# Kernel optimization log

Hardware: AMD Instinct MI355X
Metric: run time of the kernel (lower is better)

Reference implementation:

```python
import jax, jax.numpy as jnp
import numpy as np

D_MODEL = 512
D_STATE = 64
L_SEQ = 4096
BATCH = 4


def _make_A(N):
    # HiPPO-LegS style A: A[n,k] = -sqrt(2n+1)sqrt(2k+1) if n>k, -(n+1) if n==k, 0 else (n,k from 1..N)
    idx = np.arange(1, N + 1, dtype=np.float64)
    M = np.sqrt(2 * idx[:, None] + 1) * np.sqrt(2 * idx[None, :] + 1)
    lower = (idx[:, None] > idx[None, :]).astype(np.float64)
    return -(lower * M + np.diag(idx + 1))


def _discretize(A, B, C, step):
    # bilinear (Tustin) transform
    I = np.eye(A.shape[0])
    BL = np.linalg.inv(I - step / 2.0 * A)
    Ab = BL @ (I + step / 2.0 * A)
    Bb = (BL * step) @ B
    return Ab, Bb, C


def setup_inputs() -> dict:
    key = jax.random.key(0)
    rng = np.random.RandomState(0)
    A = _make_A(D_STATE)
    B = rng.randn(D_STATE, 1)
    C = rng.randn(1, D_STATE)
    Ab, Bb, Cb = _discretize(A, B, C, step=1.0 / L_SEQ)
    u = jax.random.normal(key, (BATCH, L_SEQ, D_MODEL), dtype=jnp.float32)
    return {
        "u": u,
        "A_": jnp.asarray(Ab, dtype=jnp.float32),
        "B_": jnp.asarray(Bb, dtype=jnp.float32),
        "C_": jnp.asarray(Cb, dtype=jnp.float32),
    }


def reference(u, A_, B_, C_):
    # u: (B, L, D) -> flatten channels: (BD, L)
    b, L, d = u.shape
    uc = u.transpose(0, 2, 1).reshape(b * d, L)
    N = A_.shape[0]
    b_vec = B_[:, 0]  # (N,)
    c_vec = C_[0]     # (N,)

    def step(x, u_k):
        # x: (BD, N), u_k: (BD,)
        # x_k = A_ @ x_{k-1}^T + B_ @ u_k^T  (expressed batched as x @ A_.T + outer)
        x_new = x @ A_.T + u_k[:, None] * b_vec[None, :]
        y_k = x_new @ c_vec  # (BD,)
        return x_new, y_k

    x0 = jnp.zeros((b * d, N), dtype=u.dtype)
    _, ys = jax.lax.scan(step, x0, uc.T)  # ys: (L, BD)
    y = ys.T.reshape(b, d, L).transpose(0, 2, 1)  # (B, L, D)
    return y
```

## Files before the change

### kernel.cpp

```cpp
#include <hip/hip_runtime.h>

#define L_SEQ   4096
#define D_MODEL 512
#define NSEQ    2048
#define CH      128
#define NC      32

#define OFF_P    0
#define OFF_W1T  4096
#define OFF_WOUT 12288
#define OFF_KLOC 20480
#define OFF_GX   20736

#define BC(v, j) __int_as_float(__builtin_amdgcn_readlane(__float_as_int(v), (j)))

__global__ __launch_bounds__(256) void k_prep(
    const float* __restrict__ A, const float* __restrict__ B,
    const float* __restrict__ C, float* __restrict__ ws) {
  __shared__ float Srow[64][68];
  __shared__ float STs[64][68];
  __shared__ float vrT[128][68];
  __shared__ float cwS[129][68];
  __shared__ float Cs[64], Bsh[64];

  const int tid = threadIdx.x;
  if (tid < 64) { Cs[tid] = C[tid]; Bsh[tid] = B[tid]; }
  for (int e = tid; e < 4096; e += 256) {
    const float a = A[e];
    Srow[e >> 6][e & 63] = a;
    STs[e & 63][e >> 6] = a;
  }
  __syncthreads();

  if (tid < 64) {
    vrT[0][tid] = Bsh[tid];
    float acc = 0.f;
#pragma unroll
    for (int k = 0; k < 64; ++k) acc += Cs[k] * STs[tid][k];
    cwS[1][tid] = acc;
  }
  __syncthreads();

  const int iy4 = (tid >> 4) * 4, jx4 = (tid & 15) * 4;

  for (int t = 0; t < 7; ++t) {
    const int nd = 1 << t;

    if (nd <= 2) {
      const int total = 2 * nd * 64;
      if (tid < total) {
        const int half = (tid >= nd * 64);
        const int o = (tid >> 6) & (nd - 1);
        const int idx = tid & 63;
        float acc = 0.f;
        if (!half) {
#pragma unroll
          for (int k = 0; k < 64; ++k) acc += vrT[o][k] * Srow[idx][k];
          vrT[nd + o][idx] = acc;
        } else {
#pragma unroll
          for (int k = 0; k < 64; ++k) acc += cwS[1 + o][k] * STs[idx][k];
          cwS[nd + 1 + o][idx] = acc;
        }
      }
    } else {
      const int tilesPerGemm = nd * 4;
      for (int tt = tid; tt < 2 * tilesPerGemm; tt += 256) {
        const int half = (tt >= tilesPerGemm);
        const int q = half ? tt - tilesPerGemm : tt;
        const int m0 = (q >> 4) * 4;
        const int i0 = (q & 15) * 4;
        float acc[4][4] = {{0.f}};
        if (!half) {
#pragma unroll 4
          for (int k = 0; k < 64; k += 4) {
            float a_[4][4];
#pragma unroll
            for (int r = 0; r < 4; ++r)
              *(float4*)&a_[r][0] = *(const float4*)&vrT[m0 + r][k];
#pragma unroll
            for (int kk = 0; kk < 4; ++kk) {
              const float4 b4 = *(const float4*)&STs[k + kk][i0];
#pragma unroll
              for (int r = 0; r < 4; ++r) {
                const float av = a_[r][kk];
                acc[r][0] += av * b4.x; acc[r][1] += av * b4.y;
                acc[r][2] += av * b4.z; acc[r][3] += av * b4.w;
              }
            }
          }
#pragma unroll
          for (int r = 0; r < 4; ++r) {
            float4 v; v.x = acc[r][0]; v.y = acc[r][1]; v.z = acc[r][2]; v.w = acc[r][3];
            *(float4*)&vrT[nd + m0 + r][i0] = v;
          }
        } else {
#pragma unroll 4
          for (int k = 0; k < 64; k += 4) {
            float a_[4][4];
#pragma unroll
            for (int r = 0; r < 4; ++r)
              *(float4*)&a_[r][0] = *(const float4*)&cwS[1 + m0 + r][k];
#pragma unroll
            for (int kk = 0; kk < 4; ++kk) {
              const float4 b4 = *(const float4*)&Srow[k + kk][i0];
#pragma unroll
              for (int r = 0; r < 4; ++r) {
                const float av = a_[r][kk];
                acc[r][0] += av * b4.x; acc[r][1] += av * b4.y;
                acc[r][2] += av * b4.z; acc[r][3] += av * b4.w;
              }
            }
          }
#pragma unroll
          for (int r = 0; r < 4; ++r) {
            float4 v; v.x = acc[r][0]; v.y = acc[r][1]; v.z = acc[r][2]; v.w = acc[r][3];
            *(float4*)&cwS[nd + 1 + m0 + r][i0] = v;
          }
        }
      }
    }

    float sacc[4][4] = {{0.f}};
#pragma unroll 4
    for (int k = 0; k < 64; k += 4) {
      float a_[4][4];
#pragma unroll
      for (int r = 0; r < 4; ++r)
        *(float4*)&a_[r][0] = *(const float4*)&Srow[iy4 + r][k];
#pragma unroll
      for (int kk = 0; kk < 4; ++kk) {
        const float4 b4 = *(const float4*)&Srow[k + kk][jx4];
#pragma unroll
        for (int r = 0; r < 4; ++r) {
          const float av = a_[r][kk];
          sacc[r][0] += av * b4.x; sacc[r][1] += av * b4.y;
          sacc[r][2] += av * b4.z; sacc[r][3] += av * b4.w;
        }
      }
    }
    __syncthreads();
#pragma unroll
    for (int r = 0; r < 4; ++r) {
      float4 v; v.x = sacc[r][0]; v.y = sacc[r][1]; v.z = sacc[r][2]; v.w = sacc[r][3];
      *(float4*)&Srow[iy4 + r][jx4] = v;
    }
#pragma unroll
    for (int c = 0; c < 4; ++c) {
      float4 v; v.x = sacc[0][c]; v.y = sacc[1][c]; v.z = sacc[2][c]; v.w = sacc[3][c];
      *(float4*)&STs[jx4 + c][iy4] = v;
    }
    __syncthreads();
  }

  float* Pg = ws + OFF_P;
  for (int e = tid; e < 4096; e += 256) Pg[e] = Srow[e >> 6][e & 63];

  float* W1Tg = ws + OFF_W1T;
  for (int e = tid; e < 8192; e += 256) W1Tg[e] = vrT[127 - (e >> 6)][e & 63];

  float* Wg = ws + OFF_WOUT;
  for (int e = tid; e < 8192; e += 256) Wg[e] = cwS[(e & 127) + 1][e >> 7];

  float* Kz = ws + OFF_KLOC;
  if (tid < 128) {
    float acc = 0.f;
#pragma unroll
    for (int i = 0; i < 64; ++i) acc += Cs[i] * vrT[tid][i];
    Kz[128 + tid] = acc;
  } else {
    Kz[tid - 128] = 0.f;
  }
}

__global__ __launch_bounds__(256) void k_proj(
    const float* __restrict__ u, const float* __restrict__ wsr,
    float* __restrict__ gx) {
  __shared__ float W1s[128][66];
  __shared__ float Us[64][132];

  const int st = blockIdx.x;
  const int c = blockIdx.y;
  const int tid = threadIdx.x;
  const int sgl = st * 128;
  const int bi = sgl >> 9, d0 = sgl & 511;

  const float* W1Tg = wsr + OFF_W1T;
#pragma unroll
  for (int k = 0; k < 32; ++k) {
    const int e = tid + 256 * k;
    W1s[e >> 6][e & 63] = W1Tg[e];
  }

  const float* ub = u + ((size_t)bi * L_SEQ + c * CH) * D_MODEL + d0;
  const int sy4 = (tid >> 3) * 4;
  const int ix8 = (tid & 7) * 8;

  float acc[4][8];
#pragma unroll
  for (int r = 0; r < 4; ++r)
#pragma unroll
    for (int cc = 0; cc < 8; ++cc) acc[r][cc] = 0.f;

  for (int h = 0; h < 2; ++h) {
    __syncthreads();
#pragma unroll
    for (int e8 = 0; e8 < 8; ++e8) {
      const int e = tid + 256 * e8;
      const int rr = e >> 5, s4 = (e & 31) * 4;
      *(float4*)&Us[rr][s4] =
          *(const float4*)(ub + (size_t)(h * 64 + rr) * D_MODEL + s4);
    }
    __syncthreads();
#pragma unroll 4
    for (int rr = 0; rr < 64; ++rr) {
      const int r = h * 64 + rr;
      const float4 a = *(const float4*)&Us[rr][sy4];
      const float4 b0 = *(const float4*)&W1s[r][ix8];
      const float4 b1 = *(const float4*)&W1s[r][ix8 + 4];
      acc[0][0] += a.x * b0.x; acc[0][1] += a.x * b0.y; acc[0][2] += a.x * b0.z; acc[0][3] += a.x * b0.w;
      acc[0][4] += a.x * b1.x; acc[0][5] += a.x * b1.y; acc[0][6] += a.x * b1.z; acc[0][7] += a.x * b1.w;
      acc[1][0] += a.y * b0.x; acc[1][1] += a.y * b0.y; acc[1][2] += a.y * b0.z; acc[1][3] += a.y * b0.w;
      acc[1][4] += a.y * b1.x; acc[1][5] += a.y * b1.y; acc[1][6] += a.y * b1.z; acc[1][7] += a.y * b1.w;
      acc[2][0] += a.z * b0.x; acc[2][1] += a.z * b0.y; acc[2][2] += a.z * b0.z; acc[2][3] += a.z * b0.w;
      acc[2][4] += a.z * b1.x; acc[2][5] += a.z * b1.y; acc[2][6] += a.z * b1.z; acc[2][7] += a.z * b1.w;
      acc[3][0] += a.w * b0.x; acc[3][1] += a.w * b0.y; acc[3][2] += a.w * b0.z; acc[3][3] += a.w * b0.w;
      acc[3][4] += a.w * b1.x; acc[3][5] += a.w * b1.y; acc[3][6] += a.w * b1.z; acc[3][7] += a.w * b1.w;
    }
  }

  float* gb = gx + ((size_t)c * NSEQ + sgl) * 64;
#pragma unroll
  for (int as = 0; as < 4; ++as) {
    float4 v0, v1;
    v0.x = acc[as][0]; v0.y = acc[as][1]; v0.z = acc[as][2]; v0.w = acc[as][3];
    v1.x = acc[as][4]; v1.y = acc[as][5]; v1.z = acc[as][6]; v1.w = acc[as][7];
    float* row = gb + (size_t)(sy4 + as) * 64 + ix8;
    *(float4*)row = v0;
    *(float4*)(row + 4) = v1;
  }
}

__global__ __launch_bounds__(256) void k_scan(
    const float* __restrict__ wsr, float* __restrict__ gx) {
  const int lane = threadIdx.x & 63, wv = threadIdx.x >> 6;
  const int s = blockIdx.x * 4 + wv;

  float p[64];
  {
    const float* pr = wsr + OFF_P + lane * 64;
#pragma unroll
    for (int j = 0; j < 64; j += 4) {
      const float4 v = *(const float4*)(pr + j);
      p[j] = v.x; p[j + 1] = v.y; p[j + 2] = v.z; p[j + 3] = v.w;
    }
  }

  const size_t CS = (size_t)NSEQ * 64;
  float* gs = gx + (size_t)s * 64 + lane;
  float x = 0.f;
  float g0 = gs[0];
  float g1 = gs[CS];
  float g2 = gs[2 * CS];
  for (int c = 0; c < NC; ++c) {
    const float gn = (c + 3 < NC) ? gs[(size_t)(c + 3) * CS] : 0.f;
    gs[(size_t)c * CS] = x;
    float x0 = g0, x1 = 0.f;
#pragma unroll
    for (int j = 0; j < 64; j += 2) {
      x0 += p[j] * BC(x, j);
      x1 += p[j + 1] * BC(x, j + 1);
    }
    x = x0 + x1;
    g0 = g1; g1 = g2; g2 = gn;
  }
}

__global__ __launch_bounds__(256) void k_localout(
    const float* __restrict__ u, const float* __restrict__ wsr,
    const float* __restrict__ gx, float* __restrict__ out) {
  __shared__ float As[64][132];
  __shared__ float Bs[64][132];

  const int sg = blockIdx.x;
  const int c = blockIdx.y;
  const int sgl = sg * 128;
  const int bi = sgl >> 9, d0 = sgl & 511;

  const float* KlocZ = wsr + OFF_KLOC;
  const float* WoutG = wsr + OFF_WOUT;
  const float* ub = u + ((size_t)bi * L_SEQ + c * CH) * D_MODEL + d0;

  const int tid = threadIdx.x;
  const int lane = tid & 63, w = tid >> 6;
  const int ry8 = (w * 4 + (lane >> 4)) * 8;
  const int sx4 = (lane & 15) * 4;

  float acc[8][8];
#pragma unroll
  for (int r = 0; r < 8; ++r)
#pragma unroll
    for (int cc = 0; cc < 8; ++cc) acc[r][cc] = 0.f;

  for (int kt = 0; kt < 2; ++kt) {
    const int k0 = kt * 64;
#pragma unroll
    for (int e8 = 0; e8 < 8; ++e8) {
      const int e = tid + 256 * e8;
      const int kk = e >> 5, s4 = (e & 31) * 4;
      *(float4*)&Bs[kk][s4] = *(const float4*)(ub + (size_t)(k0 + kk) * D_MODEL + s4);
    }
    const int base = 128 - k0;
#pragma unroll
    for (int e4 = 0; e4 < 32; ++e4) {
      const int e = tid + 256 * e4;
      const int kk = e >> 7, r = e & 127;
      As[kk][r] = KlocZ[base + r - kk];
    }
    __syncthreads();
    if (kt == 0 || ry8 >= 64) {
#pragma unroll 8
      for (int kk = 0; kk < 64; ++kk) {
        const float4 a0 = *(const float4*)&As[kk][ry8];
        const float4 a1 = *(const float4*)&As[kk][ry8 + 4];
        const float4 b0 = *(const float4*)&Bs[kk][sx4];
        const float4 b1 = *(const float4*)&Bs[kk][64 + sx4];
        const float av[8] = {a0.x, a0.y, a0.z, a0.w, a1.x, a1.y, a1.z, a1.w};
        const float bv[8] = {b0.x, b0.y, b0.z, b0.w, b1.x, b1.y, b1.z, b1.w};
#pragma unroll
        for (int ii = 0; ii < 8; ++ii)
#pragma unroll
          for (int jj = 0; jj < 8; ++jj) acc[ii][jj] += av[ii] * bv[jj];
      }
    }
    __syncthreads();
  }

  {
    const float* xc = gx + ((size_t)c * NSEQ + sgl) * 64;
#pragma unroll
    for (int e8 = 0; e8 < 8; ++e8) {
      const int e = tid + 256 * e8;
      const int sl = e >> 4, i4 = (e & 15) * 4;
      const float4 v = *(const float4*)(xc + (size_t)sl * 64 + i4);
      Bs[i4 + 0][sl] = v.x;
      Bs[i4 + 1][sl] = v.y;
      Bs[i4 + 2][sl] = v.z;
      Bs[i4 + 3][sl] = v.w;
    }
#pragma unroll
    for (int e4 = 0; e4 < 8; ++e4) {
      const int e = tid + 256 * e4;
      const int i_ = e >> 5, r4 = (e & 31) * 4;
      *(float4*)&As[i_][r4] = *(const float4*)(WoutG + i_ * 128 + r4);
    }
    __syncthreads();
#pragma unroll 8
    for (int kk = 0; kk < 64; ++kk) {
      const float4 a0 = *(const float4*)&As[kk][ry8];
      const float4 a1 = *(const float4*)&As[kk][ry8 + 4];
      const float4 b0 = *(const float4*)&Bs[kk][sx4];
      const float4 b1 = *(const float4*)&Bs[kk][64 + sx4];
      const float av[8] = {a0.x, a0.y, a0.z, a0.w, a1.x, a1.y, a1.z, a1.w};
      const float bv[8] = {b0.x, b0.y, b0.z, b0.w, b1.x, b1.y, b1.z, b1.w};
#pragma unroll
      for (int ii = 0; ii < 8; ++ii)
#pragma unroll
        for (int jj = 0; jj < 8; ++jj) acc[ii][jj] += av[ii] * bv[jj];
    }
  }

  float* ob = out + ((size_t)bi * L_SEQ + c * CH) * D_MODEL + d0;
#pragma unroll
  for (int r = 0; r < 8; ++r) {
    float4 v0, v1;
    v0.x = acc[r][0]; v0.y = acc[r][1]; v0.z = acc[r][2]; v0.w = acc[r][3];
    v1.x = acc[r][4]; v1.y = acc[r][5]; v1.z = acc[r][6]; v1.w = acc[r][7];
    float* row = ob + (size_t)(ry8 + r) * D_MODEL;
    *(float4*)(row + sx4) = v0;
    *(float4*)(row + 64 + sx4) = v1;
  }
}

extern "C" void kernel_launch(void* const* d_in, const int* in_sizes, int n_in,
                              void* d_out, int out_size, void* d_ws,
                              size_t ws_size, hipStream_t stream) {
  const float* u = (const float*)d_in[0];
  const float* A = (const float*)d_in[1];
  const float* B = (const float*)d_in[2];
  const float* C = (const float*)d_in[3];
  float* out = (float*)d_out;
  float* ws = (float*)d_ws;
  float* gx = ws + OFF_GX;

  k_prep<<<1, 256, 0, stream>>>(A, B, C, ws);
  k_proj<<<dim3(16, 32), 256, 0, stream>>>(u, ws, gx);
  k_scan<<<512, 256, 0, stream>>>(ws, gx);
  k_localout<<<dim3(16, 32), 256, 0, stream>>>(u, ws, gx, out);
}
```

Baseline: 201.7 us.

## Halve sequence tile width and read Toeplitz kernel from precomputed shifted copies

Both k_proj and k_localout now work on 64-channel tiles instead of 128, which doubles the grid to 1024 blocks and shrinks per-thread accumulators and LDS use. The aim is better occupancy and wave count on the device. k_prep now writes four pre-shifted, zero-padded copies of the local Toeplitz kernel. k_localout loads these into LDS once and reads them with aligned float4 loads indexed by kk&3, replacing the per-tile scalar gather that built a 64x128 Toeplitz tile. The trade-off is less register-level reuse per thread and more redundant loads of W1/Wout per block.

```diff
diff --git a/kernel.cpp b/kernel.cpp
--- a/kernel.cpp
+++ b/kernel.cpp
@@ -10,7 +10,8 @@
 #define OFF_W1T  4096
 #define OFF_WOUT 12288
 #define OFF_KLOC 20480
-#define OFF_GX   20736
+#define OFF_KZS  20736
+#define OFF_GX   21760
 
 #define BC(v, j) __int_as_float(__builtin_amdgcn_readlane(__float_as_int(v), (j)))
 
@@ -22,6 +23,7 @@
   __shared__ float vrT[128][68];
   __shared__ float cwS[129][68];
   __shared__ float Cs[64], Bsh[64];
+  __shared__ float KzSh[256];
 
   const int tid = threadIdx.x;
   if (tid < 64) { Cs[tid] = C[tid]; Bsh[tid] = B[tid]; }
@@ -167,77 +169,79 @@
     float acc = 0.f;
 #pragma unroll
     for (int i = 0; i < 64; ++i) acc += Cs[i] * vrT[tid][i];
+    KzSh[128 + tid] = acc;
     Kz[128 + tid] = acc;
   } else {
+    KzSh[tid - 128] = 0.f;
     Kz[tid - 128] = 0.f;
+  }
+  __syncthreads();
+
+  float* KzSg = ws + OFF_KZS;
+  for (int e = tid; e < 1024; e += 256) {
+    const int p = e >> 8, m = e & 255;
+    KzSg[e] = (m >= p) ? KzSh[m - p] : 0.f;
   }
 }
 
 __global__ __launch_bounds__(256) void k_proj(
     const float* __restrict__ u, const float* __restrict__ wsr,
     float* __restrict__ gx) {
-  __shared__ float W1s[128][66];
-  __shared__ float Us[64][132];
+  __shared__ float W1s[128][64];
+  __shared__ float Us[64][64];
 
   const int st = blockIdx.x;
   const int c = blockIdx.y;
   const int tid = threadIdx.x;
-  const int sgl = st * 128;
+  const int sgl = st * 64;
   const int bi = sgl >> 9, d0 = sgl & 511;
 
   const float* W1Tg = wsr + OFF_W1T;
 #pragma unroll
-  for (int k = 0; k < 32; ++k) {
+  for (int k = 0; k < 8; ++k) {
     const int e = tid + 256 * k;
-    W1s[e >> 6][e & 63] = W1Tg[e];
+    const int r = e >> 4, i4 = (e & 15) * 4;
+    *(float4*)&W1s[r][i4] = *(const float4*)(W1Tg + (size_t)e * 4);
   }
 
   const float* ub = u + ((size_t)bi * L_SEQ + c * CH) * D_MODEL + d0;
-  const int sy4 = (tid >> 3) * 4;
-  const int ix8 = (tid & 7) * 8;
-
-  float acc[4][8];
+  const int sy4 = (tid >> 4) * 4;
+  const int ix4 = (tid & 15) * 4;
+
+  float acc[4][4];
 #pragma unroll
   for (int r = 0; r < 4; ++r)
 #pragma unroll
-    for (int cc = 0; cc < 8; ++cc) acc[r][cc] = 0.f;
+    for (int cc = 0; cc < 4; ++cc) acc[r][cc] = 0.f;
 
   for (int h = 0; h < 2; ++h) {
     __syncthreads();
 #pragma unroll
-    for (int e8 = 0; e8 < 8; ++e8) {
-      const int e = tid + 256 * e8;
-      const int rr = e >> 5, s4 = (e & 31) * 4;
+    for (int e4 = 0; e4 < 4; ++e4) {
+      const int e = tid + 256 * e4;
+      const int rr = e >> 4, s4 = (e & 15) * 4;
       *(float4*)&Us[rr][s4] =
           *(const float4*)(ub + (size_t)(h * 64 + rr) * D_MODEL + s4);
     }
     __syncthreads();
-#pragma unroll 4
-    for (int rr = 0; rr < 64; ++rr) {
-      const int r = h * 64 + rr;
-      const float4 a = *(const float4*)&Us[rr][sy4];
-      const float4 b0 = *(const float4*)&W1s[r][ix8];
-      const float4 b1 = *(const float4*)&W1s[r][ix8 + 4];
-      acc[0][0] += a.x * b0.x; acc[0][1] += a.x * b0.y; acc[0][2] += a.x * b0.z; acc[0][3] += a.x * b0.w;
-      acc[0][4] += a.x * b1.x; acc[0][5] += a.x * b1.y; acc[0][6] += a.x * b1.z; acc[0][7] += a.x * b1.w;
-      acc[1][0] += a.y * b0.x; acc[1][1] += a.y * b0.y; acc[1][2] += a.y * b0.z; acc[1][3] += a.y * b0.w;
-      acc[1][4] += a.y * b1.x; acc[1][5] += a.y * b1.y; acc[1][6] += a.y * b1.z; acc[1][7] += a.y * b1.w;
-      acc[2][0] += a.z * b0.x; acc[2][1] += a.z * b0.y; acc[2][2] += a.z * b0.z; acc[2][3] += a.z * b0.w;
-      acc[2][4] += a.z * b1.x; acc[2][5] += a.z * b1.y; acc[2][6] += a.z * b1.z; acc[2][7] += a.z * b1.w;
-      acc[3][0] += a.w * b0.x; acc[3][1] += a.w * b0.y; acc[3][2] += a.w * b0.z; acc[3][3] += a.w * b0.w;
-      acc[3][4] += a.w * b1.x; acc[3][5] += a.w * b1.y; acc[3][6] += a.w * b1.z; acc[3][7] += a.w * b1.w;
+#pragma unroll 8
+    for (int kk = 0; kk < 64; ++kk) {
+      const float4 a = *(const float4*)&Us[kk][sy4];
+      const float4 b = *(const float4*)&W1s[h * 64 + kk][ix4];
+      const float av[4] = {a.x, a.y, a.z, a.w};
+      const float bv[4] = {b.x, b.y, b.z, b.w};
+#pragma unroll
+      for (int ii = 0; ii < 4; ++ii)
+#pragma unroll
+        for (int jj = 0; jj < 4; ++jj) acc[ii][jj] += av[ii] * bv[jj];
     }
   }
 
   float* gb = gx + ((size_t)c * NSEQ + sgl) * 64;
 #pragma unroll
-  for (int as = 0; as < 4; ++as) {
-    float4 v0, v1;
-    v0.x = acc[as][0]; v0.y = acc[as][1]; v0.z = acc[as][2]; v0.w = acc[as][3];
-    v1.x = acc[as][4]; v1.y = acc[as][5]; v1.z = acc[as][6]; v1.w = acc[as][7];
-    float* row = gb + (size_t)(sy4 + as) * 64 + ix8;
-    *(float4*)row = v0;
-    *(float4*)(row + 4) = v1;
+  for (int j = 0; j < 4; ++j) {
+    float4 v; v.x = acc[j][0]; v.y = acc[j][1]; v.z = acc[j][2]; v.w = acc[j][3];
+    *(float4*)(gb + (size_t)(sy4 + j) * 64 + ix4) = v;
   }
 }
 
@@ -276,109 +280,104 @@
   }
 }
 
+#define LO_BS(k, s)   LDSf[(k) * 64 + (s)]
+#define LO_KZS        4096
+#define LO_ASW(i, r)  LDSf[4096 + (i) * 128 + (r)]
+
 __global__ __launch_bounds__(256) void k_localout(
     const float* __restrict__ u, const float* __restrict__ wsr,
     const float* __restrict__ gx, float* __restrict__ out) {
-  __shared__ float As[64][132];
-  __shared__ float Bs[64][132];
+  __shared__ float LDSf[12288];
 
   const int sg = blockIdx.x;
   const int c = blockIdx.y;
-  const int sgl = sg * 128;
+  const int sgl = sg * 64;
   const int bi = sgl >> 9, d0 = sgl & 511;
 
-  const float* KlocZ = wsr + OFF_KLOC;
+  const float* KzSg = wsr + OFF_KZS;
   const float* WoutG = wsr + OFF_WOUT;
   const float* ub = u + ((size_t)bi * L_SEQ + c * CH) * D_MODEL + d0;
 
   const int tid = threadIdx.x;
-  const int lane = tid & 63, w = tid >> 6;
-  const int ry8 = (w * 4 + (lane >> 4)) * 8;
-  const int sx4 = (lane & 15) * 4;
-
-  float acc[8][8];
+  const int ry8 = (tid >> 4) * 8;
+  const int sx4 = (tid & 15) * 4;
+
+  *(float4*)&LDSf[LO_KZS + tid * 4] = *(const float4*)(KzSg + tid * 4);
+
+  float acc[8][4];
 #pragma unroll
   for (int r = 0; r < 8; ++r)
 #pragma unroll
-    for (int cc = 0; cc < 8; ++cc) acc[r][cc] = 0.f;
+    for (int cc = 0; cc < 4; ++cc) acc[r][cc] = 0.f;
 
   for (int kt = 0; kt < 2; ++kt) {
     const int k0 = kt * 64;
 #pragma unroll
-    for (int e8 = 0; e8 < 8; ++e8) {
-      const int e = tid + 256 * e8;
-      const int kk = e >> 5, s4 = (e & 31) * 4;
-      *(float4*)&Bs[kk][s4] = *(const float4*)(ub + (size_t)(k0 + kk) * D_MODEL + s4);
-    }
+    for (int e4 = 0; e4 < 4; ++e4) {
+      const int e = tid + 256 * e4;
+      const int kk = e >> 4, s4 = (e & 15) * 4;
+      *(float4*)&LO_BS(kk, s4) =
+          *(const float4*)(ub + (size_t)(k0 + kk) * D_MODEL + s4);
+    }
+    __syncthreads();
     const int base = 128 - k0;
-#pragma unroll
-    for (int e4 = 0; e4 < 32; ++e4) {
-      const int e = tid + 256 * e4;
-      const int kk = e >> 7, r = e & 127;
-      As[kk][r] = KlocZ[base + r - kk];
-    }
-    __syncthreads();
     if (kt == 0 || ry8 >= 64) {
 #pragma unroll 8
       for (int kk = 0; kk < 64; ++kk) {
-        const float4 a0 = *(const float4*)&As[kk][ry8];
-        const float4 a1 = *(const float4*)&As[kk][ry8 + 4];
-        const float4 b0 = *(const float4*)&Bs[kk][sx4];
-        const float4 b1 = *(const float4*)&Bs[kk][64 + sx4];
+        const int p = kk & 3;
+        const int idx = base + ry8 - kk + p;
+        const float4 a0 = *(const float4*)&LDSf[LO_KZS + p * 256 + idx];
+        const float4 a1 = *(const float4*)&LDSf[LO_KZS + p * 256 + idx + 4];
+        const float4 b = *(const float4*)&LO_BS(kk, sx4);
         const float av[8] = {a0.x, a0.y, a0.z, a0.w, a1.x, a1.y, a1.z, a1.w};
-        const float bv[8] = {b0.x, b0.y, b0.z, b0.w, b1.x, b1.y, b1.z, b1.w};
+        const float bv[4] = {b.x, b.y, b.z, b.w};
 #pragma unroll
         for (int ii = 0; ii < 8; ++ii)
 #pragma unroll
-          for (int jj = 0; jj < 8; ++jj) acc[ii][jj] += av[ii] * bv[jj];
+          for (int jj = 0; jj < 4; ++jj) acc[ii][jj] += av[ii] * bv[jj];
       }
     }
     __syncthreads();
   }
 
   {
-    const float* xc = gx + ((size_t)c * NSEQ + sgl) * 64;
 #pragma unroll
     for (int e8 = 0; e8 < 8; ++e8) {
       const int e = tid + 256 * e8;
-      const int sl = e >> 4, i4 = (e & 15) * 4;
+      const int i_ = e >> 5, r4 = (e & 31) * 4;
+      *(float4*)&LO_ASW(i_, r4) = *(const float4*)(WoutG + i_ * 128 + r4);
+    }
+    const float* xc = gx + ((size_t)c * NSEQ + sgl) * 64;
+#pragma unroll
+    for (int e4 = 0; e4 < 4; ++e4) {
+      const int e = tid + 256 * e4;
+      const int sl = e & 63, i4 = ((e >> 6) & 15) * 4;
       const float4 v = *(const float4*)(xc + (size_t)sl * 64 + i4);
-      Bs[i4 + 0][sl] = v.x;
-      Bs[i4 + 1][sl] = v.y;
-      Bs[i4 + 2][sl] = v.z;
-      Bs[i4 + 3][sl] = v.w;
-    }
-#pragma unroll
-    for (int e4 = 0; e4 < 8; ++e4) {
-      const int e = tid + 256 * e4;
-      const int i_ = e >> 5, r4 = (e & 31) * 4;
-      *(float4*)&As[i_][r4] = *(const float4*)(WoutG + i_ * 128 + r4);
+      LO_BS(i4 + 0, sl) = v.x;
+      LO_BS(i4 + 1, sl) = v.y;
+      LO_BS(i4 + 2, sl) = v.z;
+      LO_BS(i4 + 3, sl) = v.w;
     }
     __syncthreads();
 #pragma unroll 8
     for (int kk = 0; kk < 64; ++kk) {
-      const float4 a0 = *(const float4*)&As[kk][ry8];
-      const float4 a1 = *(const float4*)&As[kk][ry8 + 4];
-      const float4 b0 = *(const float4*)&Bs[kk][sx4];
-      const float4 b1 = *(const float4*)&Bs[kk][64 + sx4];
+      const float4 a0 = *(const float4*)&LO_ASW(kk, ry8);
+      const float4 a1 = *(const float4*)&LO_ASW(kk, ry8 + 4);
+      const float4 b = *(const float4*)&LO_BS(kk, sx4);
       const float av[8] = {a0.x, a0.y, a0.z, a0.w, a1.x, a1.y, a1.z, a1.w};
-      const float bv[8] = {b0.x, b0.y, b0.z, b0.w, b1.x, b1.y, b1.z, b1.w};
+      const float bv[4] = {b.x, b.y, b.z, b.w};
 #pragma unroll
       for (int ii = 0; ii < 8; ++ii)
 #pragma unroll
-        for (int jj = 0; jj < 8; ++jj) acc[ii][jj] += av[ii] * bv[jj];
+        for (int jj = 0; jj < 4; ++jj) acc[ii][jj] += av[ii] * bv[jj];
     }
   }
 
   float* ob = out + ((size_t)bi * L_SEQ + c * CH) * D_MODEL + d0;
 #pragma unroll
   for (int r = 0; r < 8; ++r) {
-    float4 v0, v1;
-    v0.x = acc[r][0]; v0.y = acc[r][1]; v0.z = acc[r][2]; v0.w = acc[r][3];
-    v1.x = acc[r][4]; v1.y = acc[r][5]; v1.z = acc[r][6]; v1.w = acc[r][7];
-    float* row = ob + (size_t)(ry8 + r) * D_MODEL;
-    *(float4*)(row + sx4) = v0;
-    *(float4*)(row + 64 + sx4) = v1;
+    float4 v; v.x = acc[r][0]; v.y = acc[r][1]; v.z = acc[r][2]; v.w = acc[r][3];
+    *(float4*)(ob + (size_t)(ry8 + r) * D_MODEL + sx4) = v;
   }
 }
 
@@ -394,7 +393,7 @@
   float* gx = ws + OFF_GX;
 
   k_prep<<<1, 256, 0, stream>>>(A, B, C, ws);
-  k_proj<<<dim3(16, 32), 256, 0, stream>>>(u, ws, gx);
+  k_proj<<<dim3(32, 32), 256, 0, stream>>>(u, ws, gx);
   k_scan<<<512, 256, 0, stream>>>(ws, gx);
-  k_localout<<<dim3(16, 32), 256, 0, stream>>>(u, ws, gx, out);
-}
+  k_localout<<<dim3(32, 32), 256, 0, stream>>>(u, ws, gx, out);
+}
```

After: 193.3 us. -4.2%, faster.
